# Kernel tuning notes

Measured on AMD Instinct MI355X. Metric: run time of the kernel, lower is better.

Reference implementation:

```python
import jax, jax.numpy as jnp
import numpy as np

D_MODEL = 1024
D_STATE = 16
D_CONV = 4
EXPAND = 2
D_INNER = EXPAND * D_MODEL  # 2048
DT_RANK = (D_MODEL + 15) // 16  # 64
BATCH = 2
SEQ = 1024


def setup_inputs() -> dict:
    key = jax.random.key(0)
    ks = jax.random.split(key, 9)
    s = 0.02
    x = jax.random.normal(ks[0], (BATCH, SEQ, D_MODEL), jnp.float32)
    W_in = jax.random.normal(ks[1], (D_MODEL, 2 * D_INNER), jnp.float32) * s
    conv_w = jax.random.normal(ks[2], (D_INNER, D_CONV), jnp.float32) * s
    conv_b = jnp.zeros((D_INNER,), jnp.float32)
    W_x = jax.random.normal(ks[3], (D_INNER, DT_RANK + 2 * D_STATE), jnp.float32) * s
    W_dt = jax.random.normal(ks[4], (DT_RANK, D_INNER), jnp.float32) * (DT_RANK ** -0.5)
    # dt bias init: inverse softplus of dt ~ U(1e-3, 0.1)
    dt0 = jax.random.uniform(ks[5], (D_INNER,), jnp.float32, 1e-3, 0.1)
    b_dt = dt0 + jnp.log(-jnp.expm1(-dt0))
    # S4D-real A init: A[d, n] = -(n+1)
    A_log = jnp.log(jnp.tile(jnp.arange(1, D_STATE + 1, dtype=jnp.float32), (D_INNER, 1)))
    D_skip = jnp.ones((D_INNER,), jnp.float32)
    W_out = jax.random.normal(ks[6], (D_INNER, D_MODEL), jnp.float32) * s
    return {"x": x, "W_in": W_in, "conv_w": conv_w, "conv_b": conv_b,
            "W_x": W_x, "W_dt": W_dt, "b_dt": b_dt, "A_log": A_log,
            "D_skip": D_skip, "W_out": W_out}


def _mamba_forward(x, W_in, conv_w, conv_b, W_x, W_dt, b_dt, A_log, D_skip, W_out):
    Bsz, L, _ = x.shape
    # input projection -> [B, L, 2*d_inner], split into stream and gate
    xz = x @ W_in
    xr, z = jnp.split(xz, 2, axis=-1)
    # depthwise causal conv1d over time
    xt = xr.transpose(0, 2, 1)                       # [B, d_inner, L]
    kern = conv_w[:, None, :]                        # [d_inner, 1, d_conv]
    xc = jax.lax.conv_general_dilated(
        xt, kern, window_strides=(1,), padding=[(D_CONV - 1, 0)],
        feature_group_count=D_INNER, dimension_numbers=("NCH", "OIH", "NCH"))
    xc = jax.nn.silu(xc + conv_b[None, :, None]).transpose(0, 2, 1)  # [B, L, d_inner]
    # data-dependent dt, B, C
    dbl = xc @ W_x                                   # [B, L, dt_rank + 2*d_state]
    dt, Bm, Cm = jnp.split(dbl, [DT_RANK, DT_RANK + D_STATE], axis=-1)
    dt = jax.nn.softplus(dt @ W_dt + b_dt)           # [B, L, d_inner]
    A = -jnp.exp(A_log)                              # [d_inner, d_state]

    def step(h, inp):
        dt_t, B_t, C_t, x_t = inp                    # [B,d_inner],[B,d_state],[B,d_state],[B,d_inner]
        dA = jnp.exp(dt_t[..., None] * A)            # [B, d_inner, d_state]
        h = dA * h + (dt_t * x_t)[..., None] * B_t[:, None, :]
        y = jnp.einsum("bds,bs->bd", h, C_t)
        return h, y

    h0 = jnp.zeros((Bsz, D_INNER, D_STATE), x.dtype)
    xs = (dt.transpose(1, 0, 2), Bm.transpose(1, 0, 2),
          Cm.transpose(1, 0, 2), xc.transpose(1, 0, 2))
    _, ys = jax.lax.scan(step, h0, xs)               # ys: [L, B, d_inner]
    y = ys.transpose(1, 0, 2) + xc * D_skip
    y = y * jax.nn.silu(z)
    return y @ W_out                                 # [B, L, d_model]


def reference(x, W_in, conv_w, conv_b, W_x, W_dt, b_dt, A_log, D_skip, W_out):
    return _mamba_forward(x, W_in, conv_w, conv_b, W_x, W_dt, b_dt, A_log, D_skip, W_out)
```

## Files before the change

kernel.cpp:

```cpp
#include <hip/hip_runtime.h>

#define BATCH 2
#define SEQL 1024
#define DMODEL 1024
#define DINNER 2048
#define DSTATE 16
#define DTRANK 64
#define NCH 64
#define LC 16

typedef short bf16x8 __attribute__((ext_vector_type(8)));
typedef float f32x4 __attribute__((ext_vector_type(4)));
typedef int i32x4 __attribute__((ext_vector_type(4)));

__device__ __forceinline__ unsigned short f2bf(float f) {
  unsigned u = __float_as_uint(f);
  return (unsigned short)((u + 0x7fffu + ((u >> 16) & 1u)) >> 16);
}
__device__ __forceinline__ float bf2f(unsigned short u) {
  return __uint_as_float((unsigned)u << 16);
}
__device__ __forceinline__ float sigmoidf_(float x) { return 1.f / (1.f + __expf(-x)); }

__device__ __forceinline__ void gl_lds16(const unsigned short* g, unsigned short* l) {
  __builtin_amdgcn_global_load_lds(
      (const __attribute__((address_space(1))) unsigned int*)g,
      (__attribute__((address_space(3))) unsigned int*)l, 16, 0, 0);
}

#define BM 128
#define BN 128

__global__ __launch_bounds__(256) void k_gemm_mfma(
    const unsigned short* __restrict__ A,
    const unsigned short* __restrict__ Bt,
    float* __restrict__ C, unsigned short* __restrict__ C2,
    int M, int N, int K, const float* __restrict__ bias, int mode)
{
  __shared__ __attribute__((aligned(16))) unsigned short As[128 * 64];
  __shared__ __attribute__((aligned(16))) unsigned short Bs[128 * 64];
  const int tid = threadIdx.x;
  const int wave = tid >> 6, lane = tid & 63;
  const int m0 = blockIdx.x * BM, n0 = blockIdx.y * BN;
  const int Kc = K / gridDim.z;
  const int k0beg = blockIdx.z * Kc;
  float* Cz = C + (size_t)blockIdx.z * M * N;
  const int wr = (wave >> 1) * 64, wc = (wave & 1) * 64;
  const int fr = lane & 15;
  const int qw = lane >> 4;

  int srow[4], scol[4];
  #pragma unroll
  for (int i = 0; i < 4; ++i) {
    int off = wave * 4096 + i * 1024 + lane * 16;
    int row = off >> 7;
    int c16 = ((off >> 4) & 7) ^ (row & 7);
    srow[i] = row;
    scol[i] = c16 * 8;
  }

  f32x4 acc[4][4] = {};
  for (int k0 = k0beg; k0 < k0beg + Kc; k0 += 64) {
    #pragma unroll
    for (int i = 0; i < 4; ++i)
      gl_lds16(A + (size_t)(m0 + srow[i]) * K + k0 + scol[i],
               &As[(wave * 4096 + i * 1024) >> 1]);
    #pragma unroll
    for (int i = 0; i < 4; ++i)
      gl_lds16(Bt + (size_t)(n0 + srow[i]) * K + k0 + scol[i],
               &Bs[(wave * 4096 + i * 1024) >> 1]);
    __syncthreads();
    #pragma unroll
    for (int t = 0; t < 2; ++t) {
      bf16x8 af[4], bfv[4];
      #pragma unroll
      for (int i = 0; i < 4; ++i) {
        int row = wr + i * 16 + fr;
        int c16 = (t * 4 + qw) ^ (row & 7);
        af[i] = *(const bf16x8*)&As[row * 64 + c16 * 8];
      }
      #pragma unroll
      for (int j = 0; j < 4; ++j) {
        int row = wc + j * 16 + fr;
        int c16 = (t * 4 + qw) ^ (row & 7);
        bfv[j] = *(const bf16x8*)&Bs[row * 64 + c16 * 8];
      }
      #pragma unroll
      for (int i = 0; i < 4; ++i)
        #pragma unroll
        for (int j = 0; j < 4; ++j)
          acc[i][j] = __builtin_amdgcn_mfma_f32_16x16x32_bf16(af[i], bfv[j], acc[i][j], 0, 0, 0);
    }
    __syncthreads();
  }
  const int rr = qw * 4;
  if (mode == 1) {
    #pragma unroll
    for (int j = 0; j < 4; ++j) {
      float bj = bias[n0 + wc + j * 16 + fr];
      #pragma unroll
      for (int i = 0; i < 4; ++i)
        #pragma unroll
        for (int r = 0; r < 4; ++r) {
          float v = acc[i][j][r] + bj;
          C2[(size_t)(m0 + wr + i * 16 + rr + r) * N + (n0 + wc + j * 16 + fr)] =
              f2bf(__logf(1.f + __expf(v)));
        }
    }
  } else if (mode == 2) {
    if (n0 < 2048) {
      #pragma unroll
      for (int i = 0; i < 4; ++i)
        #pragma unroll
        for (int j = 0; j < 4; ++j)
          #pragma unroll
          for (int r = 0; r < 4; ++r)
            C[(size_t)(m0 + wr + i * 16 + rr + r) * 2048 + (n0 + wc + j * 16 + fr)] =
                acc[i][j][r];
    } else {
      #pragma unroll
      for (int i = 0; i < 4; ++i)
        #pragma unroll
        for (int j = 0; j < 4; ++j)
          #pragma unroll
          for (int r = 0; r < 4; ++r)
            C2[(size_t)(m0 + wr + i * 16 + rr + r) * 2048 + (n0 - 2048 + wc + j * 16 + fr)] =
                f2bf(acc[i][j][r]);
    }
  } else {
    #pragma unroll
    for (int i = 0; i < 4; ++i)
      #pragma unroll
      for (int j = 0; j < 4; ++j)
        #pragma unroll
        for (int r = 0; r < 4; ++r)
          Cz[(size_t)(m0 + wr + i * 16 + rr + r) * N + (n0 + wc + j * 16 + fr)] = acc[i][j][r];
  }
}

__device__ __forceinline__ void transpose_tile(
    const float* __restrict__ src, unsigned short* __restrict__ dst,
    int R, int C, int bx, int by, float* t )
{
  int bc = bx * 64, br = by * 64;
  int tr = threadIdx.x >> 2;
  int tc = (threadIdx.x & 3) * 16;
  #pragma unroll
  for (int i = 0; i < 4; ++i) {
    float4 v = *(const float4*)(src + (size_t)(br + tr) * C + bc + tc + i * 4);
    t[tr * 65 + tc + i * 4 + 0] = v.x; t[tr * 65 + tc + i * 4 + 1] = v.y;
    t[tr * 65 + tc + i * 4 + 2] = v.z; t[tr * 65 + tc + i * 4 + 3] = v.w;
  }
  __syncthreads();
  unsigned short tmp[16];
  #pragma unroll
  for (int i = 0; i < 16; ++i) tmp[i] = f2bf(t[(tc + i) * 65 + tr]);
  unsigned short* dp = dst + (size_t)(bc + tr) * R + br + tc;
  *(i32x4*)dp = *(i32x4*)&tmp[0];
  *(i32x4*)(dp + 8) = *(i32x4*)&tmp[8];
}

__global__ __launch_bounds__(256) void k_prep(
    const float* __restrict__ x,   unsigned short* __restrict__ xbf,
    const float* __restrict__ Win, unsigned short* __restrict__ wint,
    const float* __restrict__ Wout,unsigned short* __restrict__ woutt,
    const float* __restrict__ Wdt, unsigned short* __restrict__ wdtt,
    const float* __restrict__ Wx,  unsigned short* __restrict__ wxt)
{
  __shared__ float t[64 * 65];
  int bid = blockIdx.x;
  if (bid < 1024) {
    int i = (bid * 256 + threadIdx.x) * 8;
    float4 a = *(const float4*)(x + i);
    float4 b = *(const float4*)(x + i + 4);
    unsigned short tmp[8] = {f2bf(a.x), f2bf(a.y), f2bf(a.z), f2bf(a.w),
                             f2bf(b.x), f2bf(b.y), f2bf(b.z), f2bf(b.w)};
    *(i32x4*)(xbf + i) = *(i32x4*)tmp;
  } else if (bid < 2048) {
    int tt = bid - 1024;
    transpose_tile(Win, wint, 1024, 4096, tt & 63, tt >> 6, t);
  } else if (bid < 2560) {
    int tt = bid - 2048;
    transpose_tile(Wout, woutt, 2048, 1024, tt & 15, tt >> 4, t);
  } else if (bid < 2592) {
    int tt = bid - 2560;
    transpose_tile(Wdt, wdtt, 64, 2048, tt, 0, t);
  } else {
    int idx = (bid - 2592) * 256 + threadIdx.x;
    int k = idx & (DINNER - 1);
    int n = idx >> 11;
    float v = (n < 96) ? Wx[(size_t)k * 96 + n] : 0.f;
    wxt[idx] = f2bf(v);
  }
}

__global__ __launch_bounds__(256) void k_conv_silu(
    const float* __restrict__ xr, const float* __restrict__ cw,
    const float* __restrict__ cb, unsigned short* __restrict__ xcb)
{
  int idx = blockIdx.x * 256 + threadIdx.x;
  int d = idx & (DINNER - 1);
  int bl = idx >> 11;
  int l = bl & (SEQL - 1);
  float s = cb[d];
  #pragma unroll
  for (int k = 0; k < 4; ++k) {
    int ll = l - 3 + k;
    if (ll >= 0) s += xr[(size_t)(bl - 3 + k) * DINNER + d] * cw[d * 4 + k];
  }
  float r = s * sigmoidf_(s);
  xcb[idx] = f2bf(r);
}

__global__ void k_reduce2(const float* __restrict__ part, float* __restrict__ dbl,
                          unsigned short* __restrict__ dtraw)
{
  int idx = blockIdx.x * 256 + threadIdx.x;
  float s = 0.f;
  #pragma unroll
  for (int z = 0; z < 16; ++z) s += part[(size_t)z * 2048 * 128 + idx];
  dbl[idx] = s;
  int col = idx & 127, rw = idx >> 7;
  if (col < 64) dtraw[rw * 64 + col] = f2bf(s);
}

__global__ void k_reduce5(const float* __restrict__ part, float* __restrict__ out)
{
  int idx = (blockIdx.x * 256 + threadIdx.x) * 4;
  f32x4 s = *(const f32x4*)(part + idx);
  #pragma unroll
  for (int z = 1; z < 4; ++z)
    s += *(const f32x4*)(part + (size_t)z * 2048 * 1024 + idx);
  *(f32x4*)(out + idx) = s;
}

__global__ __launch_bounds__(256) void k_scan_A(
    const unsigned short* __restrict__ dtb, const unsigned short* __restrict__ xcb,
    const float* __restrict__ dbl, const float* __restrict__ Alog,
    float2* __restrict__ hpair)
{
  __shared__ __attribute__((aligned(16))) float bcB[LC][DSTATE];
  int gid = blockIdx.x * 256 + threadIdx.x;
  int d = gid & (DINNER - 1);
  int t = gid >> 11;
  int c = t & (NCH - 1);
  int b = t >> 6;
  const int r0 = b * SEQL + c * LC;
  bcB[threadIdx.x >> 4][threadIdx.x & 15] =
      dbl[(size_t)(r0 + (threadIdx.x >> 4)) * 128 + 64 + (threadIdx.x & 15)];
  float As[DSTATE];
  #pragma unroll
  for (int i = 0; i < 4; ++i) {
    f32x4 a = *(const f32x4*)&Alog[d * DSTATE + i * 4];
    #pragma unroll
    for (int j = 0; j < 4; ++j) As[i * 4 + j] = -__expf(a[j]);
  }
  __syncthreads();
  float h[DSTATE];
  #pragma unroll
  for (int s = 0; s < DSTATE; ++s) h[s] = 0.f;
  float sumdt = 0.f;
  #pragma unroll
  for (int li = 0; li < LC; li += 2) {
    float dt0 = bf2f(dtb[(size_t)(r0 + li) * DINNER + d]);
    float xv0 = bf2f(xcb[(size_t)(r0 + li) * DINNER + d]);
    float dt1 = bf2f(dtb[(size_t)(r0 + li + 1) * DINNER + d]);
    float xv1 = bf2f(xcb[(size_t)(r0 + li + 1) * DINNER + d]);
    f32x4 B0[4], B1[4];
    #pragma unroll
    for (int i = 0; i < 4; ++i) B0[i] = *(const f32x4*)&bcB[li][i * 4];
    #pragma unroll
    for (int i = 0; i < 4; ++i) B1[i] = *(const f32x4*)&bcB[li + 1][i * 4];
    float dtx0 = dt0 * xv0, dtx1 = dt1 * xv1;
    sumdt += dt0 + dt1;
    const float* Bv0 = (const float*)B0;
    const float* Bv1 = (const float*)B1;
    #pragma unroll
    for (int s = 0; s < DSTATE; ++s) {
      float dA0 = __expf(dt0 * As[s]);
      h[s] = dA0 * h[s] + dtx0 * Bv0[s];
      float dA1 = __expf(dt1 * As[s]);
      h[s] = dA1 * h[s] + dtx1 * Bv1[s];
    }
  }
  size_t base = ((size_t)(b * NCH + c) * DSTATE) * DINNER + d;
  #pragma unroll
  for (int s = 0; s < DSTATE; ++s) {
    float2 v; v.x = h[s]; v.y = __expf(sumdt * As[s]);
    hpair[base + (size_t)s * DINNER] = v;
  }
}

__global__ void k_scan_B(const float2* __restrict__ hpair, float* __restrict__ hin)
{
  int gid = blockIdx.x * 256 + threadIdx.x;
  int d = gid & (DINNER - 1);
  int s = (gid >> 11) & (DSTATE - 1);
  int b = gid >> 15;
  float h = 0.f;
  for (int c0 = 0; c0 < NCH; c0 += 8) {
    float2 v[8];
    #pragma unroll
    for (int i = 0; i < 8; ++i)
      v[i] = hpair[((size_t)(b * NCH + c0 + i) * DSTATE + s) * DINNER + d];
    #pragma unroll
    for (int i = 0; i < 8; ++i) {
      hin[((size_t)(b * NCH + c0 + i) * DSTATE + s) * DINNER + d] = h;
      h = v[i].y * h + v[i].x;
    }
  }
}

__global__ __launch_bounds__(256) void k_scan_C(
    const unsigned short* __restrict__ dtb, const unsigned short* __restrict__ xcb,
    const float* __restrict__ dbl, const float* __restrict__ Alog,
    const float* __restrict__ hin, const float* __restrict__ Dskip,
    const unsigned short* __restrict__ zb, unsigned short* __restrict__ yact)
{
  __shared__ __attribute__((aligned(16))) float bc[LC][32];
  int gid = blockIdx.x * 256 + threadIdx.x;
  int d = gid & (DINNER - 1);
  int t = gid >> 11;
  int c = t & (NCH - 1);
  int b = t >> 6;
  const int r0 = b * SEQL + c * LC;
  {
    int step = threadIdx.x >> 4, j = (threadIdx.x & 15) * 2;
    float2 v = *(const float2*)&dbl[(size_t)(r0 + step) * 128 + 64 + j];
    bc[step][j] = v.x; bc[step][j + 1] = v.y;
  }
  float As[DSTATE];
  #pragma unroll
  for (int i = 0; i < 4; ++i) {
    f32x4 a = *(const f32x4*)&Alog[d * DSTATE + i * 4];
    #pragma unroll
    for (int j = 0; j < 4; ++j) As[i * 4 + j] = -__expf(a[j]);
  }
  float h[DSTATE];
  size_t base = ((size_t)(b * NCH + c) * DSTATE) * DINNER + d;
  #pragma unroll
  for (int s = 0; s < DSTATE; ++s) h[s] = hin[base + (size_t)s * DINNER];
  const float dsk = Dskip[d];
  __syncthreads();
  #pragma unroll
  for (int li = 0; li < LC; li += 2) {
    const int r = r0 + li;
    float dt0 = bf2f(dtb[(size_t)r * DINNER + d]);
    float xv0 = bf2f(xcb[(size_t)r * DINNER + d]);
    float zv0 = bf2f(zb [(size_t)r * DINNER + d]);
    float dt1 = bf2f(dtb[(size_t)(r + 1) * DINNER + d]);
    float xv1 = bf2f(xcb[(size_t)(r + 1) * DINNER + d]);
    float zv1 = bf2f(zb [(size_t)(r + 1) * DINNER + d]);
    f32x4 B0[4], C0[4], B1[4], C1[4];
    #pragma unroll
    for (int i = 0; i < 4; ++i) B0[i] = *(const f32x4*)&bc[li][i * 4];
    #pragma unroll
    for (int i = 0; i < 4; ++i) C0[i] = *(const f32x4*)&bc[li][16 + i * 4];
    #pragma unroll
    for (int i = 0; i < 4; ++i) B1[i] = *(const f32x4*)&bc[li + 1][i * 4];
    #pragma unroll
    for (int i = 0; i < 4; ++i) C1[i] = *(const f32x4*)&bc[li + 1][16 + i * 4];
    const float* Bv0 = (const float*)B0; const float* Cv0 = (const float*)C0;
    const float* Bv1 = (const float*)B1; const float* Cv1 = (const float*)C1;
    float dtx0 = dt0 * xv0, dtx1 = dt1 * xv1;
    float y0 = 0.f, y1 = 0.f;
    #pragma unroll
    for (int s = 0; s < DSTATE; ++s) {
      float dA0 = __expf(dt0 * As[s]);
      h[s] = dA0 * h[s] + dtx0 * Bv0[s];
      y0 += h[s] * Cv0[s];
      float dA1 = __expf(dt1 * As[s]);
      h[s] = dA1 * h[s] + dtx1 * Bv1[s];
      y1 += h[s] * Cv1[s];
    }
    y0 += xv0 * dsk;
    y1 += xv1 * dsk;
    float ya0 = y0 * (zv0 * sigmoidf_(zv0));
    float ya1 = y1 * (zv1 * sigmoidf_(zv1));
    yact[(size_t)r * DINNER + d] = f2bf(ya0);
    yact[(size_t)(r + 1) * DINNER + d] = f2bf(ya1);
  }
}

extern "C" void kernel_launch(void* const* d_in, const int* in_sizes, int n_in,
                              void* d_out, int out_size, void* d_ws, size_t ws_size,
                              hipStream_t stream) {
  const float* x     = (const float*)d_in[0];
  const float* Win   = (const float*)d_in[1];
  const float* cw    = (const float*)d_in[2];
  const float* cbias = (const float*)d_in[3];
  const float* Wx    = (const float*)d_in[4];
  const float* Wdt   = (const float*)d_in[5];
  const float* bdt   = (const float*)d_in[6];
  const float* Alog  = (const float*)d_in[7];
  const float* Dsk   = (const float*)d_in[8];
  const float* Wout  = (const float*)d_in[9];
  float* out = (float*)d_out;

  char* ws = (char*)d_ws;
  const size_t MB = 1 << 20;
  float*          xr    = (float*)         (ws);
  unsigned short* xbf   = (unsigned short*)(ws + 16 * MB);
  unsigned short* wint  = (unsigned short*)(ws + 20 * MB);
  unsigned short* xcb   = (unsigned short*)(ws + 28 * MB);
  unsigned short* wxt   = (unsigned short*)(ws + 36 * MB);
  float*          dbl   = (float*)         (ws + 37 * MB);
  unsigned short* dtraw = (unsigned short*)(ws + 38 * MB);
  unsigned short* wdtt  = (unsigned short*)(ws + 39 * MB);
  unsigned short* dtb16 = (unsigned short*)(ws + 40 * MB);
  unsigned short* zb    = (unsigned short*)(ws + 48 * MB);
  float2*         hpair = (float2*)        (ws + 56 * MB);
  float*          hin   = (float*)         (ws + 88 * MB);
  unsigned short* yact  = (unsigned short*)(ws + 104 * MB);
  unsigned short* woutt = (unsigned short*)(ws + 112 * MB);
  float* part2 = (float*)(ws);
  float* part5 = (float*)(ws);
  (void)ws_size; (void)in_sizes; (void)n_in; (void)out_size;

  k_prep<<<3616, 256, 0, stream>>>(x, xbf, Win, wint, Wout, woutt, Wdt, wdtt, Wx, wxt);
  k_gemm_mfma<<<dim3(16, 32, 1), 256, 0, stream>>>(xbf, wint, xr, zb, 2048, 4096, 1024, nullptr, 2);
  k_conv_silu<<<16384, 256, 0, stream>>>(xr, cw, cbias, xcb);
  k_gemm_mfma<<<dim3(16, 1, 16), 256, 0, stream>>>(xcb, wxt, part2, nullptr, 2048, 128, 2048, nullptr, 0);
  k_reduce2<<<1024, 256, 0, stream>>>(part2, dbl, dtraw);
  k_gemm_mfma<<<dim3(16, 16, 1), 256, 0, stream>>>(dtraw, wdtt, nullptr, dtb16, 2048, 2048, 64, bdt, 1);
  k_scan_A<<<1024, 256, 0, stream>>>(dtb16, xcb, dbl, Alog, hpair);
  k_scan_B<<<256, 256, 0, stream>>>(hpair, hin);
  k_scan_C<<<1024, 256, 0, stream>>>(dtb16, xcb, dbl, Alog, hin, Dsk, zb, yact);
  k_gemm_mfma<<<dim3(16, 8, 4), 256, 0, stream>>>(yact, woutt, part5, nullptr, 2048, 1024, 2048, nullptr, 0);
  k_reduce5<<<2048, 256, 0, stream>>>(part5, out);
}
```

Before: 151.5 us.

## Store xz and split-K partials in bf16, vectorize conv, swizzle GEMM tiles

```diff
diff --git a/kernel.cpp b/kernel.cpp
--- a/kernel.cpp
+++ b/kernel.cpp
@@ -41,10 +41,15 @@
   __shared__ __attribute__((aligned(16))) unsigned short Bs[128 * 64];
   const int tid = threadIdx.x;
   const int wave = tid >> 6, lane = tid & 63;
-  const int m0 = blockIdx.x * BM, n0 = blockIdx.y * BN;
+  const int gx = gridDim.x;
+  const int nwg = gx * gridDim.y;
+  const int flat = blockIdx.x + gx * blockIdx.y;
+  const int sw = (flat & 7) * (nwg >> 3) + (flat >> 3);
+  const int m0 = (sw % gx) * BM, n0 = (sw / gx) * BN;
   const int Kc = K / gridDim.z;
   const int k0beg = blockIdx.z * Kc;
   float* Cz = C + (size_t)blockIdx.z * M * N;
+  unsigned short* C2z = C2 + (size_t)blockIdx.z * M * N;
   const int wr = (wave >> 1) * 64, wc = (wave & 1) * 64;
   const int fr = lane & 15;
   const int qw = lane >> 4;
@@ -108,25 +113,23 @@
         }
     }
   } else if (mode == 2) {
-    if (n0 < 2048) {
-      #pragma unroll
-      for (int i = 0; i < 4; ++i)
+    #pragma unroll
+    for (int i = 0; i < 4; ++i)
+      #pragma unroll
+      for (int j = 0; j < 4; ++j)
         #pragma unroll
-        for (int j = 0; j < 4; ++j)
-          #pragma unroll
-          for (int r = 0; r < 4; ++r)
-            C[(size_t)(m0 + wr + i * 16 + rr + r) * 2048 + (n0 + wc + j * 16 + fr)] =
-                acc[i][j][r];
-    } else {
-      #pragma unroll
-      for (int i = 0; i < 4; ++i)
+        for (int r = 0; r < 4; ++r)
+          C2[(size_t)(m0 + wr + i * 16 + rr + r) * N + (n0 + wc + j * 16 + fr)] =
+              f2bf(acc[i][j][r]);
+  } else if (mode == 3) {
+    #pragma unroll
+    for (int i = 0; i < 4; ++i)
+      #pragma unroll
+      for (int j = 0; j < 4; ++j)
         #pragma unroll
-        for (int j = 0; j < 4; ++j)
-          #pragma unroll
-          for (int r = 0; r < 4; ++r)
-            C2[(size_t)(m0 + wr + i * 16 + rr + r) * 2048 + (n0 - 2048 + wc + j * 16 + fr)] =
-                f2bf(acc[i][j][r]);
-    }
+        for (int r = 0; r < 4; ++r)
+          C2z[(size_t)(m0 + wr + i * 16 + rr + r) * N + (n0 + wc + j * 16 + fr)] =
+              f2bf(acc[i][j][r]);
   } else {
     #pragma unroll
     for (int i = 0; i < 4; ++i)
@@ -195,21 +198,41 @@
 }
 
 __global__ __launch_bounds__(256) void k_conv_silu(
-    const float* __restrict__ xr, const float* __restrict__ cw,
+    const unsigned short* __restrict__ xzb, const float* __restrict__ cw,
     const float* __restrict__ cb, unsigned short* __restrict__ xcb)
 {
-  int idx = blockIdx.x * 256 + threadIdx.x;
-  int d = idx & (DINNER - 1);
+  int t = blockIdx.x * 256 + threadIdx.x;
+  int idx = t * 8;
+  int d0 = idx & (DINNER - 1);
   int bl = idx >> 11;
   int l = bl & (SEQL - 1);
-  float s = cb[d];
+  float s[8];
+  {
+    float4 c0 = *(const float4*)(cb + d0);
+    float4 c1 = *(const float4*)(cb + d0 + 4);
+    s[0] = c0.x; s[1] = c0.y; s[2] = c0.z; s[3] = c0.w;
+    s[4] = c1.x; s[5] = c1.y; s[6] = c1.z; s[7] = c1.w;
+  }
+  float4 w[8];
+  #pragma unroll
+  for (int i = 0; i < 8; ++i) w[i] = *(const float4*)(cw + (d0 + i) * 4);
   #pragma unroll
   for (int k = 0; k < 4; ++k) {
     int ll = l - 3 + k;
-    if (ll >= 0) s += xr[(size_t)(bl - 3 + k) * DINNER + d] * cw[d * 4 + k];
-  }
-  float r = s * sigmoidf_(s);
-  xcb[idx] = f2bf(r);
+    if (ll >= 0) {
+      bf16x8 v = *(const bf16x8*)&xzb[(size_t)(bl - 3 + k) * 4096 + d0];
+      #pragma unroll
+      for (int i = 0; i < 8; ++i)
+        s[i] += bf2f((unsigned short)v[i]) * ((const float*)&w[i])[k];
+    }
+  }
+  unsigned short o[8];
+  #pragma unroll
+  for (int i = 0; i < 8; ++i) {
+    float r = s[i] * sigmoidf_(s[i]);
+    o[i] = f2bf(r);
+  }
+  *(i32x4*)&xcb[idx] = *(i32x4*)o;
 }
 
 __global__ void k_reduce2(const float* __restrict__ part, float* __restrict__ dbl,
@@ -224,14 +247,18 @@
   if (col < 64) dtraw[rw * 64 + col] = f2bf(s);
 }
 
-__global__ void k_reduce5(const float* __restrict__ part, float* __restrict__ out)
-{
-  int idx = (blockIdx.x * 256 + threadIdx.x) * 4;
-  f32x4 s = *(const f32x4*)(part + idx);
-  #pragma unroll
-  for (int z = 1; z < 4; ++z)
-    s += *(const f32x4*)(part + (size_t)z * 2048 * 1024 + idx);
-  *(f32x4*)(out + idx) = s;
+__global__ void k_reduce5(const unsigned short* __restrict__ part, float* __restrict__ out)
+{
+  int idx = (blockIdx.x * 256 + threadIdx.x) * 8;
+  float s[8] = {};
+  #pragma unroll
+  for (int z = 0; z < 4; ++z) {
+    bf16x8 v = *(const bf16x8*)(part + (size_t)z * 2048 * 1024 + idx);
+    #pragma unroll
+    for (int i = 0; i < 8; ++i) s[i] += bf2f((unsigned short)v[i]);
+  }
+  *(f32x4*)(out + idx) = *(f32x4*)&s[0];
+  *(f32x4*)(out + idx + 4) = *(f32x4*)&s[4];
 }
 
 __global__ __launch_bounds__(256) void k_scan_A(
@@ -315,7 +342,7 @@
     const unsigned short* __restrict__ dtb, const unsigned short* __restrict__ xcb,
     const float* __restrict__ dbl, const float* __restrict__ Alog,
     const float* __restrict__ hin, const float* __restrict__ Dskip,
-    const unsigned short* __restrict__ zb, unsigned short* __restrict__ yact)
+    const unsigned short* __restrict__ xzb, unsigned short* __restrict__ yact)
 {
   __shared__ __attribute__((aligned(16))) float bc[LC][32];
   int gid = blockIdx.x * 256 + threadIdx.x;
@@ -347,10 +374,10 @@
     const int r = r0 + li;
     float dt0 = bf2f(dtb[(size_t)r * DINNER + d]);
     float xv0 = bf2f(xcb[(size_t)r * DINNER + d]);
-    float zv0 = bf2f(zb [(size_t)r * DINNER + d]);
+    float zv0 = bf2f(xzb[(size_t)r * 4096 + 2048 + d]);
     float dt1 = bf2f(dtb[(size_t)(r + 1) * DINNER + d]);
     float xv1 = bf2f(xcb[(size_t)(r + 1) * DINNER + d]);
-    float zv1 = bf2f(zb [(size_t)(r + 1) * DINNER + d]);
+    float zv1 = bf2f(xzb[(size_t)(r + 1) * 4096 + 2048 + d]);
     f32x4 B0[4], C0[4], B1[4], C1[4];
     #pragma unroll
     for (int i = 0; i < 4; ++i) B0[i] = *(const f32x4*)&bc[li][i * 4];
@@ -399,7 +426,7 @@
 
   char* ws = (char*)d_ws;
   const size_t MB = 1 << 20;
-  float*          xr    = (float*)         (ws);
+  unsigned short* xzb   = (unsigned short*)(ws);
   unsigned short* xbf   = (unsigned short*)(ws + 16 * MB);
   unsigned short* wint  = (unsigned short*)(ws + 20 * MB);
   unsigned short* xcb   = (unsigned short*)(ws + 28 * MB);
@@ -408,24 +435,23 @@
   unsigned short* dtraw = (unsigned short*)(ws + 38 * MB);
   unsigned short* wdtt  = (unsigned short*)(ws + 39 * MB);
   unsigned short* dtb16 = (unsigned short*)(ws + 40 * MB);
-  unsigned short* zb    = (unsigned short*)(ws + 48 * MB);
-  float2*         hpair = (float2*)        (ws + 56 * MB);
-  float*          hin   = (float*)         (ws + 88 * MB);
-  unsigned short* yact  = (unsigned short*)(ws + 104 * MB);
-  unsigned short* woutt = (unsigned short*)(ws + 112 * MB);
-  float* part2 = (float*)(ws);
-  float* part5 = (float*)(ws);
+  float2*         hpair = (float2*)        (ws + 48 * MB);
+  float*          hin   = (float*)         (ws + 80 * MB);
+  unsigned short* yact  = (unsigned short*)(ws + 96 * MB);
+  unsigned short* woutt = (unsigned short*)(ws + 104 * MB);
+  float*          part2 = (float*)         (ws + 108 * MB);
+  unsigned short* part5 = (unsigned short*)(ws + 124 * MB);
   (void)ws_size; (void)in_sizes; (void)n_in; (void)out_size;
 
   k_prep<<<3616, 256, 0, stream>>>(x, xbf, Win, wint, Wout, woutt, Wdt, wdtt, Wx, wxt);
-  k_gemm_mfma<<<dim3(16, 32, 1), 256, 0, stream>>>(xbf, wint, xr, zb, 2048, 4096, 1024, nullptr, 2);
-  k_conv_silu<<<16384, 256, 0, stream>>>(xr, cw, cbias, xcb);
+  k_gemm_mfma<<<dim3(16, 32, 1), 256, 0, stream>>>(xbf, wint, nullptr, xzb, 2048, 4096, 1024, nullptr, 2);
+  k_conv_silu<<<2048, 256, 0, stream>>>(xzb, cw, cbias, xcb);
   k_gemm_mfma<<<dim3(16, 1, 16), 256, 0, stream>>>(xcb, wxt, part2, nullptr, 2048, 128, 2048, nullptr, 0);
   k_reduce2<<<1024, 256, 0, stream>>>(part2, dbl, dtraw);
   k_gemm_mfma<<<dim3(16, 16, 1), 256, 0, stream>>>(dtraw, wdtt, nullptr, dtb16, 2048, 2048, 64, bdt, 1);
   k_scan_A<<<1024, 256, 0, stream>>>(dtb16, xcb, dbl, Alog, hpair);
   k_scan_B<<<256, 256, 0, stream>>>(hpair, hin);
-  k_scan_C<<<1024, 256, 0, stream>>>(dtb16, xcb, dbl, Alog, hin, Dsk, zb, yact);
-  k_gemm_mfma<<<dim3(16, 8, 4), 256, 0, stream>>>(yact, woutt, part5, nullptr, 2048, 1024, 2048, nullptr, 0);
-  k_reduce5<<<2048, 256, 0, stream>>>(part5, out);
-}
+  k_scan_C<<<1024, 256, 0, stream>>>(dtb16, xcb, dbl, Alog, hin, Dsk, xzb, yact);
+  k_gemm_mfma<<<dim3(16, 8, 4), 256, 0, stream>>>(yact, woutt, nullptr, part5, 2048, 1024, 2048, nullptr, 3);
+  k_reduce5<<<1024, 256, 0, stream>>>(part5, out);
+}
```

New measurement: 145.7 us. 3.8% less time.
